# Optimization experiments

Measured on AMD Instinct MI355X. Metric: run time of the kernel, lower is better.

Reference implementation:

```python
import jax, jax.numpy as jnp
import numpy as np

B_SZ, L, D_INNER = 2, 1024, 2048
D_STATE, DT_RANK = 16, 64


def setup_inputs() -> dict:
    key = jax.random.key(0)
    k1, k2, k3, k4 = jax.random.split(key, 4)
    x = jax.random.normal(k1, (B_SZ, L, D_INNER), dtype=jnp.float32)
    # Linear weights: torch layout (out_features, in_features); scaled ~1/sqrt(fan_in)
    W_x = jax.random.normal(k2, (DT_RANK + 2 * D_STATE, D_INNER), dtype=jnp.float32) / np.sqrt(D_INNER)
    W_dt = jax.random.normal(k3, (D_INNER, DT_RANK), dtype=jnp.float32) / np.sqrt(DT_RANK)
    b_dt = jax.random.normal(k4, (D_INNER,), dtype=jnp.float32) * 0.1
    # A_log = log(arange(1, d_state+1)) broadcast to (d_inner, d_state), as in __init__
    A_log = jnp.broadcast_to(jnp.log(jnp.arange(1, D_STATE + 1, dtype=jnp.float32)), (D_INNER, D_STATE))
    D = jnp.ones((D_INNER,), dtype=jnp.float32)
    return {"x": x, "W_x": W_x, "W_dt": W_dt, "b_dt": b_dt, "A_log": A_log, "D": D}


def reference(x, W_x, W_dt, b_dt, A_log, D):
    # x: (B, L, d_inner)
    xz = jnp.einsum('bld,kd->blk', x, W_x)                       # (B, L, dt_rank + 2*d_state)
    delta_raw = xz[..., :DT_RANK]
    B_in = xz[..., DT_RANK:DT_RANK + D_STATE]                    # (B, L, d_state)
    C_in = xz[..., DT_RANK + D_STATE:]                           # (B, L, d_state)
    delta = jax.nn.softplus(jnp.einsum('blr,dr->bld', delta_raw, W_dt) + b_dt)  # (B, L, d_inner)
    A = -jnp.exp(A_log)                                          # (d_inner, d_state), negative
    A_bar = jnp.exp(delta[..., None] * A)                        # (B, L, d_inner, d_state)
    B_bar = delta[..., None] * B_in[:, :, None, :]               # (B, L, d_inner, d_state)

    def step(h, inputs):
        A_t, Bx_t, C_t = inputs                                  # (B,d,n), (B,d,n), (B,n)
        h = A_t * h + Bx_t
        y_t = jnp.sum(h * C_t[:, None, :], axis=-1)              # (B, d_inner)
        return h, y_t

    h0 = jnp.zeros((x.shape[0], D_INNER, D_STATE), dtype=x.dtype)
    Bx = B_bar * x[..., None]                                    # (B, L, d_inner, d_state)
    # scan over L: move L to leading axis
    _, ys = jax.lax.scan(step, h0, (jnp.moveaxis(A_bar, 1, 0), jnp.moveaxis(Bx, 1, 0), jnp.moveaxis(C_in, 1, 0)))
    y = jnp.moveaxis(ys, 0, 1) + D * x                           # (B, L, d_inner)
    return y
```

## Files before the change

kernel.cpp:

```cpp
#include <hip/hip_runtime.h>
#include <hip/hip_bf16.h>

#define B_SZ 2
#define LSEQ 1024
#define DIN  2048
#define DST  16
#define DTR  64
#define KTOT 96
#define NROW (B_SZ * LSEQ)
#define NCH  128
#define TCH  8
#define KSP  16

__device__ __forceinline__ float b2f(unsigned int u) {
    union { unsigned int i; float f; } v;
    v.i = (u & 0xffffu) << 16;
    return v.f;
}

__device__ __forceinline__ float ldf(const void* p, size_t i, bool f32) {
    return f32 ? ((const float*)p)[i] : b2f(((const unsigned short*)p)[i]);
}

__device__ __forceinline__ float4 ld4(const void* p, size_t i, bool f32) {
    if (f32) return *(const float4*)((const float*)p + i);
    const uint2 u = *(const uint2*)((const unsigned short*)p + i);
    float4 v;
    v.x = b2f(u.x); v.y = b2f(u.x >> 16);
    v.z = b2f(u.y); v.w = b2f(u.y >> 16);
    return v;
}

__device__ __forceinline__ float softplus_f(float v) {
    return (v > 20.f) ? v : log1pf(__expf(v));
}

__global__ __launch_bounds__(256) void k_detect(const void* __restrict__ x,
                                                int* __restrict__ flag) {
    __shared__ int cnt;
    if (threadIdx.x == 0) cnt = 0;
    __syncthreads();
    const unsigned short* u = (const unsigned short*)x;
    int my = 0;
    for (int i = threadIdx.x; i < 4096; i += 256) {
        unsigned short v = u[2 * i];
        float af = fabsf(b2f(v));
        if (v == 0 || (af >= 6.0e-8f && af <= 1.7e7f)) my++;
    }
    atomicAdd(&cnt, my);
    __syncthreads();
    if (threadIdx.x == 0) *flag = (cnt < 2048) ? 1 : 0;
}

__global__ __launch_bounds__(256, 4) void k_proj(
    const void* __restrict__ x,
    const void* __restrict__ Wx,
    const int*  __restrict__ flag,
    float* __restrict__ part)
{
    const bool f32 = (*flag != 0);
    __shared__ float lx[32][68];
    __shared__ float lw[32][100];
    const int tid = threadIdx.x;
    const int bx = blockIdx.x;
    const int by = blockIdx.y;
    const int rt = tid >> 4, ct = tid & 15;
    const int r0 = rt * 4, c0 = ct * 6;

    float acc[4][6];
    #pragma unroll
    for (int i = 0; i < 4; i++)
        #pragma unroll
        for (int k = 0; k < 6; k++) acc[i][k] = 0.f;

    for (int sub = 0; sub < 4; sub++) {
        const int k0 = by * 128 + sub * 32;
        #pragma unroll
        for (int it = 0; it < 2; it++) {
            const int idx = tid + it * 256;
            const int r = idx >> 3, q = idx & 7;
            float4 v = ld4(x, (size_t)(bx * 64 + r) * DIN + k0 + q * 4, f32);
            lx[q * 4 + 0][r] = v.x; lx[q * 4 + 1][r] = v.y;
            lx[q * 4 + 2][r] = v.z; lx[q * 4 + 3][r] = v.w;
        }
        #pragma unroll
        for (int it = 0; it < 3; it++) {
            const int idx = tid + it * 256;
            const int c = idx >> 3, q = idx & 7;
            float4 v = ld4(Wx, (size_t)c * DIN + k0 + q * 4, f32);
            lw[q * 4 + 0][c] = v.x; lw[q * 4 + 1][c] = v.y;
            lw[q * 4 + 2][c] = v.z; lw[q * 4 + 3][c] = v.w;
        }
        __syncthreads();

        #pragma unroll 4
        for (int j = 0; j < 32; j++) {
            const float4 xa = *(const float4*)&lx[j][r0];
            const float2 w0 = *(const float2*)&lw[j][c0];
            const float2 w1 = *(const float2*)&lw[j][c0 + 2];
            const float2 w2 = *(const float2*)&lw[j][c0 + 4];
            const float xr[4] = {xa.x, xa.y, xa.z, xa.w};
            const float wc[6] = {w0.x, w0.y, w1.x, w1.y, w2.x, w2.y};
            #pragma unroll
            for (int i = 0; i < 4; i++)
                #pragma unroll
                for (int k = 0; k < 6; k++)
                    acc[i][k] += xr[i] * wc[k];
        }
        __syncthreads();
    }

    float* p = part + ((size_t)by * NROW + bx * 64 + r0) * KTOT + c0;
    #pragma unroll
    for (int i = 0; i < 4; i++) {
        float* row = p + (size_t)i * KTOT;
        *(float2*)(row)     = make_float2(acc[i][0], acc[i][1]);
        *(float2*)(row + 2) = make_float2(acc[i][2], acc[i][3]);
        *(float2*)(row + 4) = make_float2(acc[i][4], acc[i][5]);
    }
}

__global__ __launch_bounds__(256, 4) void k_comb(
    const float* __restrict__ part,
    const void* __restrict__ Alog,
    const int*  __restrict__ flag,
    float* __restrict__ drw, float* __restrict__ Bin, float* __restrict__ Cin,
    float* __restrict__ Aneg)
{
    const int idx = blockIdx.x * 256 + threadIdx.x;
    float s = 0.f;
    #pragma unroll 8
    for (int ks = 0; ks < KSP; ks++)
        s += part[(size_t)ks * NROW * KTOT + idx];
    const int r = idx / KTOT, c = idx % KTOT;
    if (c < DTR)            drw[r * DTR + c] = s;
    else if (c < DTR + DST) Bin[r * DST + (c - DTR)] = s;
    else                    Cin[r * DST + (c - DTR - DST)] = s;

    if (idx < DST * DIN) {
        const bool f32 = (*flag != 0);
        Aneg[idx] = -__expf(ldf(Alog, (size_t)idx, f32));
    }
}

__global__ __launch_bounds__(256, 4) void k_dt(
    const float* __restrict__ drw,
    const void* __restrict__ Wdt,
    const void* __restrict__ bdt,
    const int*  __restrict__ flag,
    float* __restrict__ dt)
{
    const bool f32 = (*flag != 0);
    __shared__ float la[64][68];
    __shared__ float lb[64][68];
    const int tid = threadIdx.x;
    const int r0g = blockIdx.x * 64, c0g = blockIdx.y * 64;

    #pragma unroll
    for (int it = 0; it < 4; it++) {
        const int idx = tid + it * 256;
        const int r = idx >> 4, q = idx & 15;
        float4 v = *(const float4*)(drw + (size_t)(r0g + r) * DTR + q * 4);
        la[q * 4 + 0][r] = v.x; la[q * 4 + 1][r] = v.y;
        la[q * 4 + 2][r] = v.z; la[q * 4 + 3][r] = v.w;
    }
    #pragma unroll
    for (int it = 0; it < 4; it++) {
        const int idx = tid + it * 256;
        const int c = idx >> 4, q = idx & 15;
        float4 v = ld4(Wdt, (size_t)(c0g + c) * DTR + q * 4, f32);
        lb[q * 4 + 0][c] = v.x; lb[q * 4 + 1][c] = v.y;
        lb[q * 4 + 2][c] = v.z; lb[q * 4 + 3][c] = v.w;
    }
    __syncthreads();

    const int rt = tid >> 4, ct = tid & 15;
    const int r0 = rt * 4, c0 = ct * 4;
    float acc[4][4];
    #pragma unroll
    for (int i = 0; i < 4; i++)
        #pragma unroll
        for (int k = 0; k < 4; k++) acc[i][k] = 0.f;

    #pragma unroll 8
    for (int j = 0; j < 64; j++) {
        const float4 a = *(const float4*)&la[j][r0];
        const float4 b = *(const float4*)&lb[j][c0];
        const float ar[4] = {a.x, a.y, a.z, a.w};
        const float bc[4] = {b.x, b.y, b.z, b.w};
        #pragma unroll
        for (int i = 0; i < 4; i++)
            #pragma unroll
            for (int k = 0; k < 4; k++)
                acc[i][k] += ar[i] * bc[k];
    }

    float bd[4];
    #pragma unroll
    for (int k = 0; k < 4; k++) bd[k] = ldf(bdt, (size_t)(c0g + c0 + k), f32);
    #pragma unroll
    for (int i = 0; i < 4; i++) {
        float4 o;
        o.x = softplus_f(acc[i][0] + bd[0]);
        o.y = softplus_f(acc[i][1] + bd[1]);
        o.z = softplus_f(acc[i][2] + bd[2]);
        o.w = softplus_f(acc[i][3] + bd[3]);
        *(float4*)(dt + (size_t)(r0g + r0 + i) * DIN + c0g + c0) = o;
    }
}

__global__ __launch_bounds__(256, 4) void k_scan1(
    const void* __restrict__ x,
    const float* __restrict__ dt,
    const float* __restrict__ Bin,
    const float* __restrict__ Aneg,
    const int*  __restrict__ flag,
    float* __restrict__ Pb,
    float* __restrict__ Hb)
{
    const bool f32 = (*flag != 0);
    __shared__ float Bs[TCH * DST];
    const int tid = threadIdx.x;
    const int d = blockIdx.x * 256 + tid;
    const int c = blockIdx.y;
    const int b = blockIdx.z;
    const int row0 = b * LSEQ + c * TCH;

    if (tid < TCH * DST) Bs[tid] = Bin[(size_t)row0 * DST + tid];

    float A[DST];
    #pragma unroll
    for (int sq = 0; sq < DST / 4; sq++)
        *(float4*)(A + sq * 4) = *(const float4*)(Aneg + (size_t)d * DST + sq * 4);
    __syncthreads();

    float P[DST], H[DST];
    #pragma unroll
    for (int s = 0; s < DST; s++) { P[s] = 1.f; H[s] = 0.f; }

    #pragma unroll 4
    for (int t = 0; t < TCH; t++) {
        const size_t off = (size_t)(row0 + t) * DIN + d;
        const float dtv = dt[off];
        const float xv  = ldf(x, off, f32);
        const float u   = dtv * xv;
        const float* bs = Bs + t * DST;
        #pragma unroll
        for (int s = 0; s < DST; s++) {
            const float e = __expf(dtv * A[s]);
            P[s] *= e;
            H[s] = e * H[s] + u * bs[s];
        }
    }

    const size_t base = (size_t)(b * NCH + c) * DST * DIN + d;
    #pragma unroll
    for (int s = 0; s < DST; s++) {
        Pb[base + (size_t)s * DIN] = P[s];
        Hb[base + (size_t)s * DIN] = H[s];
    }
}

__global__ __launch_bounds__(256, 4) void k_scan2(
    float* __restrict__ Pb,
    const float* __restrict__ Hb)
{
    const int idx = blockIdx.x * 256 + threadIdx.x;
    const int b   = idx / (DST * DIN);
    const int rem = idx % (DST * DIN);
    float h = 0.f;
    #pragma unroll 8
    for (int c = 0; c < NCH; c++) {
        const size_t o = (size_t)(b * NCH + c) * DST * DIN + rem;
        const float p = Pb[o], hb = Hb[o];
        Pb[o] = h;
        h = hb + p * h;
    }
}

__global__ __launch_bounds__(256, 4) void k_scan3(
    const void* __restrict__ x,
    const float* __restrict__ dt,
    const float* __restrict__ Bin,
    const float* __restrict__ Cin,
    const float* __restrict__ Aneg,
    const void* __restrict__ Dv,
    const float* __restrict__ hin,
    const int*  __restrict__ flag,
    void* __restrict__ y)
{
    const bool f32 = (*flag != 0);
    __shared__ float Bs[TCH * DST];
    __shared__ float Cs[TCH * DST];
    const int tid = threadIdx.x;
    const int d = blockIdx.x * 256 + tid;
    const int c = blockIdx.y;
    const int b = blockIdx.z;
    const int row0 = b * LSEQ + c * TCH;

    if (tid < TCH * DST) {
        Bs[tid] = Bin[(size_t)row0 * DST + tid];
        Cs[tid] = Cin[(size_t)row0 * DST + tid];
    }

    float A[DST];
    #pragma unroll
    for (int sq = 0; sq < DST / 4; sq++)
        *(float4*)(A + sq * 4) = *(const float4*)(Aneg + (size_t)d * DST + sq * 4);
    const float Dd = ldf(Dv, (size_t)d, f32);
    __syncthreads();

    float h[DST];
    const size_t base = (size_t)(b * NCH + c) * DST * DIN + d;
    #pragma unroll
    for (int s = 0; s < DST; s++) h[s] = hin[base + (size_t)s * DIN];

    #pragma unroll 4
    for (int t = 0; t < TCH; t++) {
        const size_t off = (size_t)(row0 + t) * DIN + d;
        const float dtv = dt[off];
        const float xv  = ldf(x, off, f32);
        const float u   = dtv * xv;
        const float* bs = Bs + t * DST;
        const float* cs = Cs + t * DST;
        float yv = Dd * xv;
        #pragma unroll
        for (int s = 0; s < DST; s++) {
            const float e = __expf(dtv * A[s]);
            h[s] = e * h[s] + u * bs[s];
            yv += h[s] * cs[s];
        }
        if (f32) ((float*)y)[off] = yv;
        else     ((__hip_bfloat16*)y)[off] = __float2bfloat16(yv);
    }
}

extern "C" void kernel_launch(void* const* d_in, const int* in_sizes, int n_in,
                              void* d_out, int out_size, void* d_ws, size_t ws_size,
                              hipStream_t stream) {
    const void* x    = d_in[0];
    const void* Wx   = d_in[1];
    const void* Wdt  = d_in[2];
    const void* bdt  = d_in[3];
    const void* Alog = d_in[4];
    const void* Dv   = d_in[5];

    int*   flag  = (int*)d_ws;
    float* basep = (float*)d_ws + 16;
    float* drw   = basep;
    float* Bin   = drw + (size_t)NROW * DTR;
    float* Cin   = Bin + (size_t)NROW * DST;
    float* Aneg  = Cin + (size_t)NROW * DST;
    float* part  = Aneg + (size_t)DIN * DST;
    float* dt    = part + (size_t)KSP * NROW * KTOT;
    float* Pb    = dt + (size_t)NROW * DIN;
    float* Hb    = Pb + (size_t)B_SZ * NCH * DST * DIN;

    k_detect<<<1, 256, 0, stream>>>(x, flag);

    k_proj<<<dim3(NROW / 64, KSP), 256, 0, stream>>>(x, Wx, flag, part);

    k_comb<<<(NROW * KTOT) / 256, 256, 0, stream>>>(part, Alog, flag,
                                                    drw, Bin, Cin, Aneg);

    k_dt<<<dim3(NROW / 64, DIN / 64), 256, 0, stream>>>(drw, Wdt, bdt, flag, dt);

    dim3 g1(DIN / 256, NCH, B_SZ);
    k_scan1<<<g1, 256, 0, stream>>>(x, dt, Bin, Aneg, flag, Pb, Hb);

    k_scan2<<<(B_SZ * DST * DIN) / 256, 256, 0, stream>>>(Pb, Hb);

    k_scan3<<<g1, 256, 0, stream>>>(x, dt, Bin, Cin, Aneg, Dv, Pb, flag, d_out);
}
```

Baseline: 183.4 us.

## Fuse pipeline stages into one cooperative persistent kernel with grid syncs

Merges the projection, combine, dt GEMM and three scan phases into a single cooperative kernel of 512 blocks separated by grid.sync(), so the separate kernel launches between phases go away. It also changes the scan chunking from 128 chunks of 8 steps to 32 chunks of 32 steps and moves the chunk state to a per-chain layout, which gives longer sequential work per block and a smaller carry pass. The cooperative launch needs all 512 blocks to be co-resident, and it falls back to the separate kernels if the launch fails. Fewer scan blocks and grid-wide barriers may leave the GPU underused during the scan phases.

```diff
diff --git a/kernel.cpp b/kernel.cpp
--- a/kernel.cpp
+++ b/kernel.cpp
@@ -1,5 +1,8 @@
 #include <hip/hip_runtime.h>
 #include <hip/hip_bf16.h>
+#include <hip/hip_cooperative_groups.h>
+
+namespace cg = cooperative_groups;
 
 #define B_SZ 2
 #define LSEQ 1024
@@ -8,9 +11,11 @@
 #define DTR  64
 #define KTOT 96
 #define NROW (B_SZ * LSEQ)
-#define NCH  128
-#define TCH  8
+#define NCH  32
+#define TCH  32
 #define KSP  16
+#define NCHAINS 16
+#define NBLK 512
 
 __device__ __forceinline__ float b2f(unsigned int u) {
     union { unsigned int i; float f; } v;
@@ -35,35 +40,14 @@
     return (v > 20.f) ? v : log1pf(__expf(v));
 }
 
-__global__ __launch_bounds__(256) void k_detect(const void* __restrict__ x,
-                                                int* __restrict__ flag) {
-    __shared__ int cnt;
-    if (threadIdx.x == 0) cnt = 0;
-    __syncthreads();
-    const unsigned short* u = (const unsigned short*)x;
-    int my = 0;
-    for (int i = threadIdx.x; i < 4096; i += 256) {
-        unsigned short v = u[2 * i];
-        float af = fabsf(b2f(v));
-        if (v == 0 || (af >= 6.0e-8f && af <= 1.7e7f)) my++;
-    }
-    atomicAdd(&cnt, my);
-    __syncthreads();
-    if (threadIdx.x == 0) *flag = (cnt < 2048) ? 1 : 0;
-}
-
-__global__ __launch_bounds__(256, 4) void k_proj(
-    const void* __restrict__ x,
-    const void* __restrict__ Wx,
-    const int*  __restrict__ flag,
-    float* __restrict__ part)
-{
-    const bool f32 = (*flag != 0);
-    __shared__ float lx[32][68];
-    __shared__ float lw[32][100];
-    const int tid = threadIdx.x;
-    const int bx = blockIdx.x;
-    const int by = blockIdx.y;
+
+__device__ __forceinline__ void phase_proj(
+    int bx, int by, int tid, bool f32,
+    const void* __restrict__ x, const void* __restrict__ Wx,
+    float* __restrict__ part, float* smem)
+{
+    float* lx = smem;
+    float* lw = smem + 32 * 68;
     const int rt = tid >> 4, ct = tid & 15;
     const int r0 = rt * 4, c0 = ct * 6;
 
@@ -80,25 +64,25 @@
             const int idx = tid + it * 256;
             const int r = idx >> 3, q = idx & 7;
             float4 v = ld4(x, (size_t)(bx * 64 + r) * DIN + k0 + q * 4, f32);
-            lx[q * 4 + 0][r] = v.x; lx[q * 4 + 1][r] = v.y;
-            lx[q * 4 + 2][r] = v.z; lx[q * 4 + 3][r] = v.w;
+            lx[(q * 4 + 0) * 68 + r] = v.x; lx[(q * 4 + 1) * 68 + r] = v.y;
+            lx[(q * 4 + 2) * 68 + r] = v.z; lx[(q * 4 + 3) * 68 + r] = v.w;
         }
         #pragma unroll
         for (int it = 0; it < 3; it++) {
             const int idx = tid + it * 256;
             const int c = idx >> 3, q = idx & 7;
             float4 v = ld4(Wx, (size_t)c * DIN + k0 + q * 4, f32);
-            lw[q * 4 + 0][c] = v.x; lw[q * 4 + 1][c] = v.y;
-            lw[q * 4 + 2][c] = v.z; lw[q * 4 + 3][c] = v.w;
+            lw[(q * 4 + 0) * 100 + c] = v.x; lw[(q * 4 + 1) * 100 + c] = v.y;
+            lw[(q * 4 + 2) * 100 + c] = v.z; lw[(q * 4 + 3) * 100 + c] = v.w;
         }
         __syncthreads();
 
         #pragma unroll 4
         for (int j = 0; j < 32; j++) {
-            const float4 xa = *(const float4*)&lx[j][r0];
-            const float2 w0 = *(const float2*)&lw[j][c0];
-            const float2 w1 = *(const float2*)&lw[j][c0 + 2];
-            const float2 w2 = *(const float2*)&lw[j][c0 + 4];
+            const float4 xa = *(const float4*)&lx[j * 68 + r0];
+            const float2 w0 = *(const float2*)&lw[j * 100 + c0];
+            const float2 w1 = *(const float2*)&lw[j * 100 + c0 + 2];
+            const float2 w2 = *(const float2*)&lw[j * 100 + c0 + 4];
             const float xr[4] = {xa.x, xa.y, xa.z, xa.w};
             const float wc[6] = {w0.x, w0.y, w1.x, w1.y, w2.x, w2.y};
             #pragma unroll
@@ -120,57 +104,49 @@
     }
 }
 
-__global__ __launch_bounds__(256, 4) void k_comb(
-    const float* __restrict__ part,
-    const void* __restrict__ Alog,
-    const int*  __restrict__ flag,
+__device__ __forceinline__ void phase_comb(
+    int g, bool f32,
+    const float* __restrict__ part, const void* __restrict__ Alog,
     float* __restrict__ drw, float* __restrict__ Bin, float* __restrict__ Cin,
     float* __restrict__ Aneg)
 {
-    const int idx = blockIdx.x * 256 + threadIdx.x;
     float s = 0.f;
     #pragma unroll 8
     for (int ks = 0; ks < KSP; ks++)
-        s += part[(size_t)ks * NROW * KTOT + idx];
-    const int r = idx / KTOT, c = idx % KTOT;
+        s += part[(size_t)ks * NROW * KTOT + g];
+    const int r = g / KTOT, c = g % KTOT;
     if (c < DTR)            drw[r * DTR + c] = s;
     else if (c < DTR + DST) Bin[r * DST + (c - DTR)] = s;
     else                    Cin[r * DST + (c - DTR - DST)] = s;
 
-    if (idx < DST * DIN) {
-        const bool f32 = (*flag != 0);
-        Aneg[idx] = -__expf(ldf(Alog, (size_t)idx, f32));
-    }
-}
-
-__global__ __launch_bounds__(256, 4) void k_dt(
-    const float* __restrict__ drw,
-    const void* __restrict__ Wdt,
-    const void* __restrict__ bdt,
-    const int*  __restrict__ flag,
-    float* __restrict__ dt)
-{
-    const bool f32 = (*flag != 0);
-    __shared__ float la[64][68];
-    __shared__ float lb[64][68];
-    const int tid = threadIdx.x;
-    const int r0g = blockIdx.x * 64, c0g = blockIdx.y * 64;
+    if (g < DST * DIN)
+        Aneg[g] = -__expf(ldf(Alog, (size_t)g, f32));
+}
+
+__device__ __forceinline__ void phase_dt(
+    int tile, int tid, bool f32,
+    const float* __restrict__ drw, const void* __restrict__ Wdt,
+    const void* __restrict__ bdt, float* __restrict__ dtg, float* smem)
+{
+    const int r0g = (tile & 31) * 64, c0g = (tile >> 5) * 64;
+    float* la = smem;
+    float* lb = smem + 64 * 68;
 
     #pragma unroll
     for (int it = 0; it < 4; it++) {
         const int idx = tid + it * 256;
         const int r = idx >> 4, q = idx & 15;
         float4 v = *(const float4*)(drw + (size_t)(r0g + r) * DTR + q * 4);
-        la[q * 4 + 0][r] = v.x; la[q * 4 + 1][r] = v.y;
-        la[q * 4 + 2][r] = v.z; la[q * 4 + 3][r] = v.w;
+        la[(q * 4 + 0) * 68 + r] = v.x; la[(q * 4 + 1) * 68 + r] = v.y;
+        la[(q * 4 + 2) * 68 + r] = v.z; la[(q * 4 + 3) * 68 + r] = v.w;
     }
     #pragma unroll
     for (int it = 0; it < 4; it++) {
         const int idx = tid + it * 256;
         const int c = idx >> 4, q = idx & 15;
         float4 v = ld4(Wdt, (size_t)(c0g + c) * DTR + q * 4, f32);
-        lb[q * 4 + 0][c] = v.x; lb[q * 4 + 1][c] = v.y;
-        lb[q * 4 + 2][c] = v.z; lb[q * 4 + 3][c] = v.w;
+        lb[(q * 4 + 0) * 68 + c] = v.x; lb[(q * 4 + 1) * 68 + c] = v.y;
+        lb[(q * 4 + 2) * 68 + c] = v.z; lb[(q * 4 + 3) * 68 + c] = v.w;
     }
     __syncthreads();
 
@@ -184,8 +160,8 @@
 
     #pragma unroll 8
     for (int j = 0; j < 64; j++) {
-        const float4 a = *(const float4*)&la[j][r0];
-        const float4 b = *(const float4*)&lb[j][c0];
+        const float4 a = *(const float4*)&la[j * 68 + r0];
+        const float4 b = *(const float4*)&lb[j * 68 + c0];
         const float ar[4] = {a.x, a.y, a.z, a.w};
         const float bc[4] = {b.x, b.y, b.z, b.w};
         #pragma unroll
@@ -205,32 +181,29 @@
         o.y = softplus_f(acc[i][1] + bd[1]);
         o.z = softplus_f(acc[i][2] + bd[2]);
         o.w = softplus_f(acc[i][3] + bd[3]);
-        *(float4*)(dt + (size_t)(r0g + r0 + i) * DIN + c0g + c0) = o;
-    }
-}
-
-__global__ __launch_bounds__(256, 4) void k_scan1(
-    const void* __restrict__ x,
-    const float* __restrict__ dt,
-    const float* __restrict__ Bin,
-    const float* __restrict__ Aneg,
-    const int*  __restrict__ flag,
-    float* __restrict__ Pb,
-    float* __restrict__ Hb)
-{
-    const bool f32 = (*flag != 0);
-    __shared__ float Bs[TCH * DST];
-    const int tid = threadIdx.x;
-    const int d = blockIdx.x * 256 + tid;
-    const int c = blockIdx.y;
-    const int b = blockIdx.z;
+        *(float4*)(dtg + (size_t)(r0g + r0 + i) * DIN + c0g + c0) = o;
+    }
+    __syncthreads();
+}
+
+__device__ __forceinline__ void phase_scan1(
+    int chain, int c, int tid, bool f32,
+    const void* __restrict__ x, const float* __restrict__ dtg,
+    const float* __restrict__ Bin, const float* __restrict__ Aneg,
+    float* __restrict__ Pb, float* __restrict__ Hb, float* smem)
+{
+    float* Bs = smem;
+    const int b = chain >> 3, dblock = chain & 7;
+    const int d = dblock * 256 + tid;
     const int row0 = b * LSEQ + c * TCH;
 
-    if (tid < TCH * DST) Bs[tid] = Bin[(size_t)row0 * DST + tid];
+    #pragma unroll
+    for (int i = 0; i < 2; i++)
+        Bs[tid + i * 256] = Bin[(size_t)row0 * DST + tid + i * 256];
 
     float A[DST];
     #pragma unroll
-    for (int sq = 0; sq < DST / 4; sq++)
+    for (int sq = 0; sq < 4; sq++)
         *(float4*)(A + sq * 4) = *(const float4*)(Aneg + (size_t)d * DST + sq * 4);
     __syncthreads();
 
@@ -241,98 +214,202 @@
     #pragma unroll 4
     for (int t = 0; t < TCH; t++) {
         const size_t off = (size_t)(row0 + t) * DIN + d;
-        const float dtv = dt[off];
-        const float xv  = ldf(x, off, f32);
-        const float u   = dtv * xv;
-        const float* bs = Bs + t * DST;
-        #pragma unroll
-        for (int s = 0; s < DST; s++) {
-            const float e = __expf(dtv * A[s]);
-            P[s] *= e;
-            H[s] = e * H[s] + u * bs[s];
+        const float dtt = dtg[off];
+        const float u   = dtt * ldf(x, off, f32);
+        #pragma unroll
+        for (int sq = 0; sq < 4; sq++) {
+            const float4 bq = *(const float4*)&Bs[t * DST + sq * 4];
+            const float bb[4] = {bq.x, bq.y, bq.z, bq.w};
+            #pragma unroll
+            for (int r = 0; r < 4; r++) {
+                const int s = sq * 4 + r;
+                const float e = __expf(dtt * A[s]);
+                P[s] *= e;
+                H[s] = e * H[s] + u * bb[r];
+            }
         }
     }
 
-    const size_t base = (size_t)(b * NCH + c) * DST * DIN + d;
+    const size_t pidx = ((size_t)chain * NCH + c) * (DST * 256) + tid;
     #pragma unroll
     for (int s = 0; s < DST; s++) {
-        Pb[base + (size_t)s * DIN] = P[s];
-        Hb[base + (size_t)s * DIN] = H[s];
-    }
-}
-
-__global__ __launch_bounds__(256, 4) void k_scan2(
-    float* __restrict__ Pb,
-    const float* __restrict__ Hb)
-{
-    const int idx = blockIdx.x * 256 + threadIdx.x;
-    const int b   = idx / (DST * DIN);
-    const int rem = idx % (DST * DIN);
+        Pb[pidx + (size_t)s * 256] = P[s];
+        Hb[pidx + (size_t)s * 256] = H[s];
+    }
+}
+
+__device__ __forceinline__ void phase_scan2(
+    int seq, float* __restrict__ Pb, const float* __restrict__ Hb)
+{
+    const int ch  = seq >> 12;
+    const int rem = seq & 4095;
     float h = 0.f;
     #pragma unroll 8
-    for (int c = 0; c < NCH; c++) {
-        const size_t o = (size_t)(b * NCH + c) * DST * DIN + rem;
+    for (int cc = 0; cc < NCH; cc++) {
+        const size_t o = ((size_t)ch * NCH + cc) * 4096 + rem;
         const float p = Pb[o], hb = Hb[o];
         Pb[o] = h;
         h = hb + p * h;
     }
 }
 
-__global__ __launch_bounds__(256, 4) void k_scan3(
-    const void* __restrict__ x,
-    const float* __restrict__ dt,
-    const float* __restrict__ Bin,
-    const float* __restrict__ Cin,
-    const float* __restrict__ Aneg,
-    const void* __restrict__ Dv,
-    const float* __restrict__ hin,
-    const int*  __restrict__ flag,
-    void* __restrict__ y)
-{
-    const bool f32 = (*flag != 0);
-    __shared__ float Bs[TCH * DST];
-    __shared__ float Cs[TCH * DST];
-    const int tid = threadIdx.x;
-    const int d = blockIdx.x * 256 + tid;
-    const int c = blockIdx.y;
-    const int b = blockIdx.z;
+__device__ __forceinline__ void phase_scan3(
+    int chain, int c, int tid, bool f32,
+    const void* __restrict__ x, const float* __restrict__ dtg,
+    const float* __restrict__ Bin, const float* __restrict__ Cin,
+    const float* __restrict__ Aneg, const void* __restrict__ Dv,
+    const float* __restrict__ hin, void* __restrict__ y, float* smem)
+{
+    float* Bs = smem;
+    float* Cs = smem + TCH * DST;
+    const int b = chain >> 3, dblock = chain & 7;
+    const int d = dblock * 256 + tid;
     const int row0 = b * LSEQ + c * TCH;
 
-    if (tid < TCH * DST) {
-        Bs[tid] = Bin[(size_t)row0 * DST + tid];
-        Cs[tid] = Cin[(size_t)row0 * DST + tid];
+    #pragma unroll
+    for (int i = 0; i < 2; i++) {
+        Bs[tid + i * 256] = Bin[(size_t)row0 * DST + tid + i * 256];
+        Cs[tid + i * 256] = Cin[(size_t)row0 * DST + tid + i * 256];
     }
 
     float A[DST];
     #pragma unroll
-    for (int sq = 0; sq < DST / 4; sq++)
+    for (int sq = 0; sq < 4; sq++)
         *(float4*)(A + sq * 4) = *(const float4*)(Aneg + (size_t)d * DST + sq * 4);
     const float Dd = ldf(Dv, (size_t)d, f32);
     __syncthreads();
 
     float h[DST];
-    const size_t base = (size_t)(b * NCH + c) * DST * DIN + d;
-    #pragma unroll
-    for (int s = 0; s < DST; s++) h[s] = hin[base + (size_t)s * DIN];
+    const size_t pidx = ((size_t)chain * NCH + c) * (DST * 256) + tid;
+    #pragma unroll
+    for (int s = 0; s < DST; s++) h[s] = hin[pidx + (size_t)s * 256];
 
     #pragma unroll 4
     for (int t = 0; t < TCH; t++) {
         const size_t off = (size_t)(row0 + t) * DIN + d;
-        const float dtv = dt[off];
+        const float dtt = dtg[off];
         const float xv  = ldf(x, off, f32);
-        const float u   = dtv * xv;
-        const float* bs = Bs + t * DST;
-        const float* cs = Cs + t * DST;
+        const float u   = dtt * xv;
         float yv = Dd * xv;
         #pragma unroll
-        for (int s = 0; s < DST; s++) {
-            const float e = __expf(dtv * A[s]);
-            h[s] = e * h[s] + u * bs[s];
-            yv += h[s] * cs[s];
+        for (int sq = 0; sq < 4; sq++) {
+            const float4 bq = *(const float4*)&Bs[t * DST + sq * 4];
+            const float4 cq = *(const float4*)&Cs[t * DST + sq * 4];
+            const float bb[4] = {bq.x, bq.y, bq.z, bq.w};
+            const float cc[4] = {cq.x, cq.y, cq.z, cq.w};
+            #pragma unroll
+            for (int r = 0; r < 4; r++) {
+                const int s = sq * 4 + r;
+                const float e = __expf(dtt * A[s]);
+                h[s] = e * h[s] + u * bb[r];
+                yv += h[s] * cc[r];
+            }
         }
         if (f32) ((float*)y)[off] = yv;
         else     ((__hip_bfloat16*)y)[off] = __float2bfloat16(yv);
     }
+}
+
+
+__global__ __launch_bounds__(256) void k_detect(const void* __restrict__ x,
+                                                int* __restrict__ flag) {
+    __shared__ int cnt;
+    if (threadIdx.x == 0) cnt = 0;
+    __syncthreads();
+    const unsigned short* u = (const unsigned short*)x;
+    int my = 0;
+    for (int i = threadIdx.x; i < 4096; i += 256) {
+        unsigned short v = u[2 * i];
+        float af = fabsf(b2f(v));
+        if (v == 0 || (af >= 6.0e-8f && af <= 1.7e7f)) my++;
+    }
+    atomicAdd(&cnt, my);
+    __syncthreads();
+    if (threadIdx.x == 0) *flag = (cnt < 2048) ? 1 : 0;
+}
+
+__global__ __launch_bounds__(256, 4) void k_mega(
+    const void* __restrict__ x, const void* __restrict__ Wx,
+    const void* __restrict__ Wdt, const void* __restrict__ bdt,
+    const void* __restrict__ Alog, const void* __restrict__ Dv,
+    const int* __restrict__ flag,
+    float* __restrict__ part, float* __restrict__ drw,
+    float* __restrict__ Bin, float* __restrict__ Cin,
+    float* __restrict__ Aneg, float* __restrict__ dtg,
+    float* __restrict__ Pb, float* __restrict__ Hb,
+    void* __restrict__ y)
+{
+    cg::grid_group grid = cg::this_grid();
+    __shared__ float smem[8704];
+    const int tid = threadIdx.x;
+    const int bid = blockIdx.x;
+    const bool f32 = (*flag != 0);
+
+    phase_proj(bid & 31, bid >> 5, tid, f32, x, Wx, part, smem);
+    grid.sync();
+
+    for (int g = bid * 256 + tid; g < NROW * KTOT; g += NBLK * 256)
+        phase_comb(g, f32, part, Alog, drw, Bin, Cin, Aneg);
+    grid.sync();
+
+    phase_dt(bid, tid, f32, drw, Wdt, bdt, dtg, smem);
+    __syncthreads();
+    phase_dt(bid + NBLK, tid, f32, drw, Wdt, bdt, dtg, smem);
+    grid.sync();
+
+    phase_scan1(bid >> 5, bid & 31, tid, f32, x, dtg, Bin, Aneg, Pb, Hb, smem);
+    grid.sync();
+
+    {
+        const int seq = bid * 256 + tid;
+        if (seq < NCHAINS * DST * 256) phase_scan2(seq, Pb, Hb);
+    }
+    grid.sync();
+
+    phase_scan3(bid >> 5, bid & 31, tid, f32, x, dtg, Bin, Cin, Aneg, Dv,
+                Pb, y, smem);
+}
+
+__global__ __launch_bounds__(256, 4) void k_proj(
+    const void* x, const void* Wx, const int* flag, float* part) {
+    __shared__ float smem[5376];
+    phase_proj(blockIdx.x, blockIdx.y, threadIdx.x, *flag != 0, x, Wx, part, smem);
+}
+
+__global__ __launch_bounds__(256, 4) void k_comb(
+    const float* part, const void* Alog, const int* flag,
+    float* drw, float* Bin, float* Cin, float* Aneg) {
+    const int g = blockIdx.x * 256 + threadIdx.x;
+    if (g < NROW * KTOT)
+        phase_comb(g, *flag != 0, part, Alog, drw, Bin, Cin, Aneg);
+}
+
+__global__ __launch_bounds__(256, 4) void k_dt(
+    const float* drw, const void* Wdt, const void* bdt, const int* flag,
+    float* dtg) {
+    __shared__ float smem[8704];
+    phase_dt(blockIdx.x, threadIdx.x, *flag != 0, drw, Wdt, bdt, dtg, smem);
+}
+
+__global__ __launch_bounds__(256, 4) void k_scan1(
+    const void* x, const float* dtg, const float* Bin, const float* Aneg,
+    const int* flag, float* Pb, float* Hb) {
+    __shared__ float smem[512];
+    phase_scan1(blockIdx.x >> 5, blockIdx.x & 31, threadIdx.x, *flag != 0,
+                x, dtg, Bin, Aneg, Pb, Hb, smem);
+}
+
+__global__ __launch_bounds__(256, 4) void k_scan2(float* Pb, const float* Hb) {
+    phase_scan2(blockIdx.x * 256 + threadIdx.x, Pb, Hb);
+}
+
+__global__ __launch_bounds__(256, 4) void k_scan3(
+    const void* x, const float* dtg, const float* Bin, const float* Cin,
+    const float* Aneg, const void* Dv, const float* hin, const int* flag,
+    void* y) {
+    __shared__ float smem[1024];
+    phase_scan3(blockIdx.x >> 5, blockIdx.x & 31, threadIdx.x, *flag != 0,
+                x, dtg, Bin, Cin, Aneg, Dv, hin, y, smem);
 }
 
 extern "C" void kernel_launch(void* const* d_in, const int* in_sizes, int n_in,
@@ -344,31 +421,38 @@
     const void* bdt  = d_in[3];
     const void* Alog = d_in[4];
     const void* Dv   = d_in[5];
+    void* yv = d_out;
 
     int*   flag  = (int*)d_ws;
     float* basep = (float*)d_ws + 16;
-    float* drw   = basep;
-    float* Bin   = drw + (size_t)NROW * DTR;
-    float* Cin   = Bin + (size_t)NROW * DST;
-    float* Aneg  = Cin + (size_t)NROW * DST;
-    float* part  = Aneg + (size_t)DIN * DST;
-    float* dt    = part + (size_t)KSP * NROW * KTOT;
-    float* Pb    = dt + (size_t)NROW * DIN;
-    float* Hb    = Pb + (size_t)B_SZ * NCH * DST * DIN;
+    float* drw  = basep;
+    float* Bin  = drw  + (size_t)NROW * DTR;
+    float* Cin  = Bin  + (size_t)NROW * DST;
+    float* Aneg = Cin  + (size_t)NROW * DST;
+    float* part = Aneg + (size_t)DIN * DST;
+    float* dt   = part + (size_t)KSP * NROW * KTOT;
+    float* Pb   = dt   + (size_t)NROW * DIN;
+    float* Hb   = Pb   + (size_t)NCHAINS * NCH * DST * 256;
 
     k_detect<<<1, 256, 0, stream>>>(x, flag);
 
-    k_proj<<<dim3(NROW / 64, KSP), 256, 0, stream>>>(x, Wx, flag, part);
-
-    k_comb<<<(NROW * KTOT) / 256, 256, 0, stream>>>(part, Alog, flag,
-                                                    drw, Bin, Cin, Aneg);
-
-    k_dt<<<dim3(NROW / 64, DIN / 64), 256, 0, stream>>>(drw, Wdt, bdt, flag, dt);
-
-    dim3 g1(DIN / 256, NCH, B_SZ);
-    k_scan1<<<g1, 256, 0, stream>>>(x, dt, Bin, Aneg, flag, Pb, Hb);
-
-    k_scan2<<<(B_SZ * DST * DIN) / 256, 256, 0, stream>>>(Pb, Hb);
-
-    k_scan3<<<g1, 256, 0, stream>>>(x, dt, Bin, Cin, Aneg, Dv, Pb, flag, d_out);
-}
+    void* kargs[] = {(void*)&x, (void*)&Wx, (void*)&Wdt, (void*)&bdt,
+                     (void*)&Alog, (void*)&Dv, (void*)&flag,
+                     (void*)&part, (void*)&drw, (void*)&Bin, (void*)&Cin,
+                     (void*)&Aneg, (void*)&dt, (void*)&Pb, (void*)&Hb,
+                     (void*)&yv};
+    hipError_t err = hipLaunchCooperativeKernel(
+        (const void*)k_mega, dim3(NBLK), dim3(256), kargs, 0, stream);
+
+    if (err != hipSuccess) {
+        (void)hipGetLastError();
+        k_proj <<<dim3(32, KSP), 256, 0, stream>>>(x, Wx, flag, part);
+        k_comb <<<(NROW * KTOT) / 256, 256, 0, stream>>>(part, Alog, flag,
+                                                         drw, Bin, Cin, Aneg);
+        k_dt   <<<1024, 256, 0, stream>>>(drw, Wdt, bdt, flag, dt);
+        k_scan1<<<NCHAINS * NCH, 256, 0, stream>>>(x, dt, Bin, Aneg, flag, Pb, Hb);
+        k_scan2<<<(NCHAINS * DST * 256) / 256, 256, 0, stream>>>(Pb, Hb);
+        k_scan3<<<NCHAINS * NCH, 256, 0, stream>>>(x, dt, Bin, Cin, Aneg, Dv,
+                                                   Pb, flag, d_out);
+    }
+}
```

Result: slower. 473.4 us (+158.1%).

## Split state across thread pairs, fuse prep, atomic split-K reduction, retile scan chunks

Applied to the files above, without the earlier changes.

Replaces the split-K partial buffer and combine kernel with atomicAdd accumulation into a zeroed xz buffer, and folds the zeroing and A=-exp(A_log) into the detect kernel. The scan kernels now give each thread half of the 16 state entries, combining y with a lane shuffle. Chunks go from 128x8 to 64x16 and the chunk-state layout is blocked per 128-channel chain. This aims to cut kernel launches, partial-sum traffic and per-thread register pressure so occupancy can rise, at the cost of atomic contention, duplicated dt/x loads per pair, and nondeterministic float summation order.

```diff
diff --git a/kernel.cpp b/kernel.cpp
--- a/kernel.cpp
+++ b/kernel.cpp
@@ -8,9 +8,10 @@
 #define DTR  64
 #define KTOT 96
 #define NROW (B_SZ * LSEQ)
-#define NCH  128
-#define TCH  8
+#define NCH  64
+#define TCH  16
 #define KSP  16
+#define NCHAINS 32
 
 __device__ __forceinline__ float b2f(unsigned int u) {
     union { unsigned int i; float f; } v;
@@ -35,8 +36,10 @@
     return (v > 20.f) ? v : log1pf(__expf(v));
 }
 
-__global__ __launch_bounds__(256) void k_detect(const void* __restrict__ x,
-                                                int* __restrict__ flag) {
+__global__ __launch_bounds__(256) void k_prep(
+    const void* __restrict__ x, const void* __restrict__ Alog,
+    int* __restrict__ flag, float* __restrict__ xz, float* __restrict__ Aneg)
+{
     __shared__ int cnt;
     if (threadIdx.x == 0) cnt = 0;
     __syncthreads();
@@ -49,18 +52,28 @@
     }
     atomicAdd(&cnt, my);
     __syncthreads();
-    if (threadIdx.x == 0) *flag = (cnt < 2048) ? 1 : 0;
+    const bool f32 = (cnt < 2048);
+    if (blockIdx.x == 0 && threadIdx.x == 0) *flag = f32 ? 1 : 0;
+
+    const int g0 = blockIdx.x * 256 + threadIdx.x;
+    #pragma unroll
+    for (int it = 0; it < 3; it++) {
+        const int g = g0 + it * 65536;
+        if (g < NROW * KTOT) xz[g] = 0.f;
+    }
+    if (g0 < DST * DIN)
+        Aneg[g0] = -__expf(ldf(Alog, (size_t)g0, f32));
 }
 
 __global__ __launch_bounds__(256, 4) void k_proj(
     const void* __restrict__ x,
     const void* __restrict__ Wx,
     const int*  __restrict__ flag,
-    float* __restrict__ part)
+    float* __restrict__ xz)
 {
     const bool f32 = (*flag != 0);
-    __shared__ float lx[32][68];
-    __shared__ float lw[32][100];
+    __shared__ float lx[32 * 68];
+    __shared__ float lw[32 * 100];
     const int tid = threadIdx.x;
     const int bx = blockIdx.x;
     const int by = blockIdx.y;
@@ -80,25 +93,25 @@
             const int idx = tid + it * 256;
             const int r = idx >> 3, q = idx & 7;
             float4 v = ld4(x, (size_t)(bx * 64 + r) * DIN + k0 + q * 4, f32);
-            lx[q * 4 + 0][r] = v.x; lx[q * 4 + 1][r] = v.y;
-            lx[q * 4 + 2][r] = v.z; lx[q * 4 + 3][r] = v.w;
+            lx[(q * 4 + 0) * 68 + r] = v.x; lx[(q * 4 + 1) * 68 + r] = v.y;
+            lx[(q * 4 + 2) * 68 + r] = v.z; lx[(q * 4 + 3) * 68 + r] = v.w;
         }
         #pragma unroll
         for (int it = 0; it < 3; it++) {
             const int idx = tid + it * 256;
             const int c = idx >> 3, q = idx & 7;
             float4 v = ld4(Wx, (size_t)c * DIN + k0 + q * 4, f32);
-            lw[q * 4 + 0][c] = v.x; lw[q * 4 + 1][c] = v.y;
-            lw[q * 4 + 2][c] = v.z; lw[q * 4 + 3][c] = v.w;
+            lw[(q * 4 + 0) * 100 + c] = v.x; lw[(q * 4 + 1) * 100 + c] = v.y;
+            lw[(q * 4 + 2) * 100 + c] = v.z; lw[(q * 4 + 3) * 100 + c] = v.w;
         }
         __syncthreads();
 
         #pragma unroll 4
         for (int j = 0; j < 32; j++) {
-            const float4 xa = *(const float4*)&lx[j][r0];
-            const float2 w0 = *(const float2*)&lw[j][c0];
-            const float2 w1 = *(const float2*)&lw[j][c0 + 2];
-            const float2 w2 = *(const float2*)&lw[j][c0 + 4];
+            const float4 xa = *(const float4*)&lx[j * 68 + r0];
+            const float2 w0 = *(const float2*)&lw[j * 100 + c0];
+            const float2 w1 = *(const float2*)&lw[j * 100 + c0 + 2];
+            const float2 w2 = *(const float2*)&lw[j * 100 + c0 + 4];
             const float xr[4] = {xa.x, xa.y, xa.z, xa.w};
             const float wc[6] = {w0.x, w0.y, w1.x, w1.y, w2.x, w2.y};
             #pragma unroll
@@ -110,49 +123,25 @@
         __syncthreads();
     }
 
-    float* p = part + ((size_t)by * NROW + bx * 64 + r0) * KTOT + c0;
     #pragma unroll
     for (int i = 0; i < 4; i++) {
-        float* row = p + (size_t)i * KTOT;
-        *(float2*)(row)     = make_float2(acc[i][0], acc[i][1]);
-        *(float2*)(row + 2) = make_float2(acc[i][2], acc[i][3]);
-        *(float2*)(row + 4) = make_float2(acc[i][4], acc[i][5]);
-    }
-}
-
-__global__ __launch_bounds__(256, 4) void k_comb(
-    const float* __restrict__ part,
-    const void* __restrict__ Alog,
-    const int*  __restrict__ flag,
-    float* __restrict__ drw, float* __restrict__ Bin, float* __restrict__ Cin,
-    float* __restrict__ Aneg)
-{
-    const int idx = blockIdx.x * 256 + threadIdx.x;
-    float s = 0.f;
-    #pragma unroll 8
-    for (int ks = 0; ks < KSP; ks++)
-        s += part[(size_t)ks * NROW * KTOT + idx];
-    const int r = idx / KTOT, c = idx % KTOT;
-    if (c < DTR)            drw[r * DTR + c] = s;
-    else if (c < DTR + DST) Bin[r * DST + (c - DTR)] = s;
-    else                    Cin[r * DST + (c - DTR - DST)] = s;
-
-    if (idx < DST * DIN) {
-        const bool f32 = (*flag != 0);
-        Aneg[idx] = -__expf(ldf(Alog, (size_t)idx, f32));
+        float* row = xz + (size_t)(bx * 64 + r0 + i) * KTOT + c0;
+        #pragma unroll
+        for (int k = 0; k < 6; k++)
+            atomicAdd(row + k, acc[i][k]);
     }
 }
 
 __global__ __launch_bounds__(256, 4) void k_dt(
-    const float* __restrict__ drw,
+    const float* __restrict__ xz,
     const void* __restrict__ Wdt,
     const void* __restrict__ bdt,
     const int*  __restrict__ flag,
-    float* __restrict__ dt)
+    float* __restrict__ dtg)
 {
     const bool f32 = (*flag != 0);
-    __shared__ float la[64][68];
-    __shared__ float lb[64][68];
+    __shared__ float la[64 * 68];
+    __shared__ float lb[64 * 68];
     const int tid = threadIdx.x;
     const int r0g = blockIdx.x * 64, c0g = blockIdx.y * 64;
 
@@ -160,17 +149,17 @@
     for (int it = 0; it < 4; it++) {
         const int idx = tid + it * 256;
         const int r = idx >> 4, q = idx & 15;
-        float4 v = *(const float4*)(drw + (size_t)(r0g + r) * DTR + q * 4);
-        la[q * 4 + 0][r] = v.x; la[q * 4 + 1][r] = v.y;
-        la[q * 4 + 2][r] = v.z; la[q * 4 + 3][r] = v.w;
+        float4 v = *(const float4*)(xz + (size_t)(r0g + r) * KTOT + q * 4);
+        la[(q * 4 + 0) * 68 + r] = v.x; la[(q * 4 + 1) * 68 + r] = v.y;
+        la[(q * 4 + 2) * 68 + r] = v.z; la[(q * 4 + 3) * 68 + r] = v.w;
     }
     #pragma unroll
     for (int it = 0; it < 4; it++) {
         const int idx = tid + it * 256;
         const int c = idx >> 4, q = idx & 15;
         float4 v = ld4(Wdt, (size_t)(c0g + c) * DTR + q * 4, f32);
-        lb[q * 4 + 0][c] = v.x; lb[q * 4 + 1][c] = v.y;
-        lb[q * 4 + 2][c] = v.z; lb[q * 4 + 3][c] = v.w;
+        lb[(q * 4 + 0) * 68 + c] = v.x; lb[(q * 4 + 1) * 68 + c] = v.y;
+        lb[(q * 4 + 2) * 68 + c] = v.z; lb[(q * 4 + 3) * 68 + c] = v.w;
     }
     __syncthreads();
 
@@ -184,8 +173,8 @@
 
     #pragma unroll 8
     for (int j = 0; j < 64; j++) {
-        const float4 a = *(const float4*)&la[j][r0];
-        const float4 b = *(const float4*)&lb[j][c0];
+        const float4 a = *(const float4*)&la[j * 68 + r0];
+        const float4 b = *(const float4*)&lb[j * 68 + c0];
         const float ar[4] = {a.x, a.y, a.z, a.w};
         const float bc[4] = {b.x, b.y, b.z, b.w};
         #pragma unroll
@@ -205,84 +194,86 @@
         o.y = softplus_f(acc[i][1] + bd[1]);
         o.z = softplus_f(acc[i][2] + bd[2]);
         o.w = softplus_f(acc[i][3] + bd[3]);
-        *(float4*)(dt + (size_t)(r0g + r0 + i) * DIN + c0g + c0) = o;
-    }
-}
-
-__global__ __launch_bounds__(256, 4) void k_scan1(
+        *(float4*)(dtg + (size_t)(r0g + r0 + i) * DIN + c0g + c0) = o;
+    }
+}
+
+__global__ __launch_bounds__(256, 8) void k_scan1(
     const void* __restrict__ x,
-    const float* __restrict__ dt,
-    const float* __restrict__ Bin,
+    const float* __restrict__ dtg,
+    const float* __restrict__ xz,
     const float* __restrict__ Aneg,
     const int*  __restrict__ flag,
-    float* __restrict__ Pb,
-    float* __restrict__ Hb)
+    float* __restrict__ Pb, float* __restrict__ Hb)
 {
     const bool f32 = (*flag != 0);
     __shared__ float Bs[TCH * DST];
     const int tid = threadIdx.x;
-    const int d = blockIdx.x * 256 + tid;
-    const int c = blockIdx.y;
-    const int b = blockIdx.z;
+    const int bid = blockIdx.x;
+    const int chain = bid >> 6, c = bid & 63;
+    const int b = chain >> 4, dblk = chain & 15;
+    const int dlocal = tid >> 1, shalf = tid & 1;
+    const int d = dblk * 128 + dlocal;
     const int row0 = b * LSEQ + c * TCH;
 
-    if (tid < TCH * DST) Bs[tid] = Bin[(size_t)row0 * DST + tid];
-
-    float A[DST];
-    #pragma unroll
-    for (int sq = 0; sq < DST / 4; sq++)
-        *(float4*)(A + sq * 4) = *(const float4*)(Aneg + (size_t)d * DST + sq * 4);
-    __syncthreads();
-
-    float P[DST], H[DST];
-    #pragma unroll
-    for (int s = 0; s < DST; s++) { P[s] = 1.f; H[s] = 0.f; }
+    {
+        const int r = tid >> 4, s = tid & 15;
+        Bs[tid] = xz[(size_t)(row0 + r) * KTOT + DTR + s];
+    }
+    float A[8];
+    #pragma unroll
+    for (int q = 0; q < 2; q++)
+        *(float4*)(A + q * 4) =
+            *(const float4*)(Aneg + (size_t)d * DST + shalf * 8 + q * 4);
+    __syncthreads();
+
+    float P[8], H[8];
+    #pragma unroll
+    for (int k = 0; k < 8; k++) { P[k] = 1.f; H[k] = 0.f; }
 
     #pragma unroll 4
     for (int t = 0; t < TCH; t++) {
         const size_t off = (size_t)(row0 + t) * DIN + d;
-        const float dtv = dt[off];
-        const float xv  = ldf(x, off, f32);
-        const float u   = dtv * xv;
-        const float* bs = Bs + t * DST;
-        #pragma unroll
-        for (int s = 0; s < DST; s++) {
-            const float e = __expf(dtv * A[s]);
-            P[s] *= e;
-            H[s] = e * H[s] + u * bs[s];
-        }
-    }
-
-    const size_t base = (size_t)(b * NCH + c) * DST * DIN + d;
-    #pragma unroll
-    for (int s = 0; s < DST; s++) {
-        Pb[base + (size_t)s * DIN] = P[s];
-        Hb[base + (size_t)s * DIN] = H[s];
-    }
-}
-
-__global__ __launch_bounds__(256, 4) void k_scan2(
-    float* __restrict__ Pb,
-    const float* __restrict__ Hb)
-{
-    const int idx = blockIdx.x * 256 + threadIdx.x;
-    const int b   = idx / (DST * DIN);
-    const int rem = idx % (DST * DIN);
+        const float dtt = dtg[off];
+        const float u   = dtt * ldf(x, off, f32);
+        const float* bs = Bs + t * DST + shalf * 8;
+        #pragma unroll
+        for (int k = 0; k < 8; k++) {
+            const float e = __expf(dtt * A[k]);
+            P[k] *= e;
+            H[k] = e * H[k] + u * bs[k];
+        }
+    }
+
+    const size_t base = ((size_t)chain * NCH + c) * (DST * 128)
+                      + (size_t)shalf * 8 * 128 + dlocal;
+    #pragma unroll
+    for (int k = 0; k < 8; k++) {
+        Pb[base + (size_t)k * 128] = P[k];
+        Hb[base + (size_t)k * 128] = H[k];
+    }
+}
+
+__global__ __launch_bounds__(256, 8) void k_scan2(
+    float* __restrict__ Pb, const float* __restrict__ Hb)
+{
+    const int g = blockIdx.x * 256 + threadIdx.x;
+    const int chain = g >> 11;
+    const int rem   = g & 2047;
     float h = 0.f;
     #pragma unroll 8
-    for (int c = 0; c < NCH; c++) {
-        const size_t o = (size_t)(b * NCH + c) * DST * DIN + rem;
+    for (int cc = 0; cc < NCH; cc++) {
+        const size_t o = ((size_t)chain * NCH + cc) * 2048 + rem;
         const float p = Pb[o], hb = Hb[o];
         Pb[o] = h;
         h = hb + p * h;
     }
 }
 
-__global__ __launch_bounds__(256, 4) void k_scan3(
+__global__ __launch_bounds__(256, 8) void k_scan3(
     const void* __restrict__ x,
-    const float* __restrict__ dt,
-    const float* __restrict__ Bin,
-    const float* __restrict__ Cin,
+    const float* __restrict__ dtg,
+    const float* __restrict__ xz,
     const float* __restrict__ Aneg,
     const void* __restrict__ Dv,
     const float* __restrict__ hin,
@@ -293,45 +284,52 @@
     __shared__ float Bs[TCH * DST];
     __shared__ float Cs[TCH * DST];
     const int tid = threadIdx.x;
-    const int d = blockIdx.x * 256 + tid;
-    const int c = blockIdx.y;
-    const int b = blockIdx.z;
+    const int bid = blockIdx.x;
+    const int chain = bid >> 6, c = bid & 63;
+    const int b = chain >> 4, dblk = chain & 15;
+    const int dlocal = tid >> 1, shalf = tid & 1;
+    const int d = dblk * 128 + dlocal;
     const int row0 = b * LSEQ + c * TCH;
 
-    if (tid < TCH * DST) {
-        Bs[tid] = Bin[(size_t)row0 * DST + tid];
-        Cs[tid] = Cin[(size_t)row0 * DST + tid];
-    }
-
-    float A[DST];
-    #pragma unroll
-    for (int sq = 0; sq < DST / 4; sq++)
-        *(float4*)(A + sq * 4) = *(const float4*)(Aneg + (size_t)d * DST + sq * 4);
+    {
+        const int r = tid >> 4, s = tid & 15;
+        Bs[tid] = xz[(size_t)(row0 + r) * KTOT + DTR + s];
+        Cs[tid] = xz[(size_t)(row0 + r) * KTOT + DTR + DST + s];
+    }
+    float A[8];
+    #pragma unroll
+    for (int q = 0; q < 2; q++)
+        *(float4*)(A + q * 4) =
+            *(const float4*)(Aneg + (size_t)d * DST + shalf * 8 + q * 4);
     const float Dd = ldf(Dv, (size_t)d, f32);
     __syncthreads();
 
-    float h[DST];
-    const size_t base = (size_t)(b * NCH + c) * DST * DIN + d;
-    #pragma unroll
-    for (int s = 0; s < DST; s++) h[s] = hin[base + (size_t)s * DIN];
+    float h[8];
+    const size_t base = ((size_t)chain * NCH + c) * (DST * 128)
+                      + (size_t)shalf * 8 * 128 + dlocal;
+    #pragma unroll
+    for (int k = 0; k < 8; k++) h[k] = hin[base + (size_t)k * 128];
 
     #pragma unroll 4
     for (int t = 0; t < TCH; t++) {
         const size_t off = (size_t)(row0 + t) * DIN + d;
-        const float dtv = dt[off];
+        const float dtt = dtg[off];
         const float xv  = ldf(x, off, f32);
-        const float u   = dtv * xv;
-        const float* bs = Bs + t * DST;
-        const float* cs = Cs + t * DST;
-        float yv = Dd * xv;
-        #pragma unroll
-        for (int s = 0; s < DST; s++) {
-            const float e = __expf(dtv * A[s]);
-            h[s] = e * h[s] + u * bs[s];
-            yv += h[s] * cs[s];
-        }
-        if (f32) ((float*)y)[off] = yv;
-        else     ((__hip_bfloat16*)y)[off] = __float2bfloat16(yv);
+        const float u   = dtt * xv;
+        const float* bs = Bs + t * DST + shalf * 8;
+        const float* cs = Cs + t * DST + shalf * 8;
+        float yp = 0.f;
+        #pragma unroll
+        for (int k = 0; k < 8; k++) {
+            const float e = __expf(dtt * A[k]);
+            h[k] = e * h[k] + u * bs[k];
+            yp += h[k] * cs[k];
+        }
+        const float ytot = yp + __shfl_xor(yp, 1, 64) + Dd * xv;
+        if (shalf == 0) {
+            if (f32) ((float*)y)[off] = ytot;
+            else     ((__hip_bfloat16*)y)[off] = __float2bfloat16(ytot);
+        }
     }
 }
 
@@ -347,28 +345,22 @@
 
     int*   flag  = (int*)d_ws;
     float* basep = (float*)d_ws + 16;
-    float* drw   = basep;
-    float* Bin   = drw + (size_t)NROW * DTR;
-    float* Cin   = Bin + (size_t)NROW * DST;
-    float* Aneg  = Cin + (size_t)NROW * DST;
-    float* part  = Aneg + (size_t)DIN * DST;
-    float* dt    = part + (size_t)KSP * NROW * KTOT;
-    float* Pb    = dt + (size_t)NROW * DIN;
-    float* Hb    = Pb + (size_t)B_SZ * NCH * DST * DIN;
-
-    k_detect<<<1, 256, 0, stream>>>(x, flag);
-
-    k_proj<<<dim3(NROW / 64, KSP), 256, 0, stream>>>(x, Wx, flag, part);
-
-    k_comb<<<(NROW * KTOT) / 256, 256, 0, stream>>>(part, Alog, flag,
-                                                    drw, Bin, Cin, Aneg);
-
-    k_dt<<<dim3(NROW / 64, DIN / 64), 256, 0, stream>>>(drw, Wdt, bdt, flag, dt);
-
-    dim3 g1(DIN / 256, NCH, B_SZ);
-    k_scan1<<<g1, 256, 0, stream>>>(x, dt, Bin, Aneg, flag, Pb, Hb);
-
-    k_scan2<<<(B_SZ * DST * DIN) / 256, 256, 0, stream>>>(Pb, Hb);
-
-    k_scan3<<<g1, 256, 0, stream>>>(x, dt, Bin, Cin, Aneg, Dv, Pb, flag, d_out);
-}
+    float* xz   = basep;
+    float* Aneg = xz   + (size_t)NROW * KTOT;
+    float* dt   = Aneg + (size_t)DIN * DST;
+    float* Pb   = dt   + (size_t)NROW * DIN;
+    float* Hb   = Pb   + (size_t)NCHAINS * NCH * DST * 128;
+
+    k_prep<<<256, 256, 0, stream>>>(x, Alog, flag, xz, Aneg);
+
+    k_proj<<<dim3(NROW / 64, KSP), 256, 0, stream>>>(x, Wx, flag, xz);
+
+    k_dt<<<dim3(NROW / 64, DIN / 64), 256, 0, stream>>>(xz, Wdt, bdt, flag, dt);
+
+    k_scan1<<<NCHAINS * NCH, 256, 0, stream>>>(x, dt, xz, Aneg, flag, Pb, Hb);
+
+    k_scan2<<<(NCHAINS * DST * 128) / 256, 256, 0, stream>>>(Pb, Hb);
+
+    k_scan3<<<NCHAINS * NCH, 256, 0, stream>>>(x, dt, xz, Aneg, Dv, Pb, flag,
+                                               d_out);
+}
```

After: 242.2 us. +32.0%, slower.
